# Performance work log

Measured on AMD Instinct MI355X. Metric: run time of the kernel, lower is better.

The kernel has to match this reference:

```python
import jax, jax.numpy as jnp
import numpy as np

D_MODEL = 2048
N_HEADS = 16
D_K = D_MODEL // N_HEADS


def setup_inputs() -> dict:
    key = jax.random.key(0)
    ks = jax.random.split(key, 9)
    s = 1.0 / np.sqrt(D_MODEL)
    def lin(k):
        kw, kb = jax.random.split(k)
        W = jax.random.uniform(kw, (D_MODEL, D_MODEL), jnp.float32, -s, s)
        b = jax.random.uniform(kb, (D_MODEL,), jnp.float32, -s, s)
        return W, b
    Wq, bq = lin(ks[0])
    Wk, bk = lin(ks[1])
    Wv, bv = lin(ks[2])
    Wo, bo = lin(ks[3])
    x = jax.random.normal(ks[4], (2, 2048, D_MODEL), jnp.float32)
    return {"x": x, "Wq": Wq, "bq": bq, "Wk": Wk, "bk": bk,
            "Wv": Wv, "bv": bv, "Wo": Wo, "bo": bo}


def _mha(x, Wq, bq, Wk, bk, Wv, bv, Wo, bo):
    B, S, _ = x.shape
    # Linear projections (torch Linear: x @ W.T + b), split into heads: b s (h d) -> b h s d
    def proj(W, b):
        y = jnp.einsum('bsm,nm->bsn', x, W) + b
        return y.reshape(B, S, N_HEADS, D_K).transpose(0, 2, 1, 3)
    q = proj(Wq, bq)
    k = proj(Wk, bk)
    v = proj(Wv, bv)
    scores = jnp.einsum('bhsd,bhtd->bhst', q, k) / jnp.sqrt(jnp.float32(D_K))
    causal = jnp.triu(jnp.ones((S, S), bool), k=1)  # True above diagonal -> masked
    scores = jnp.where(causal[None, None], -jnp.inf, scores)
    attn = jax.nn.softmax(scores, axis=-1)  # dropout p=0 (eval)
    out = jnp.einsum('bhst,bhtd->bhsd', attn, v)
    out = out.transpose(0, 2, 1, 3).reshape(B, S, D_MODEL)
    return jnp.einsum('bsm,nm->bsn', out, Wo) + bo


def reference(x, Wq, bq, Wk, bk, Wv, bv, Wo, bo):
    return _mha(x, Wq, bq, Wk, bk, Wv, bv, Wo, bo)
```

## Files before the change

### kernel.cpp

```cpp
#include <hip/hip_runtime.h>

typedef unsigned short u16;
typedef __attribute__((ext_vector_type(8))) short bf16x8;
typedef __attribute__((ext_vector_type(4))) float f32x4;
typedef __attribute__((ext_vector_type(4))) unsigned short u16x4;

__device__ __forceinline__ u16 f2bf(float f) {
  union { float f; unsigned u; } v; v.f = f;
  return (u16)((v.u + 0x7FFFu + ((v.u >> 16) & 1u)) >> 16);
}

__device__ __forceinline__ void gload16(const u16* g, u16* l) {
  __builtin_amdgcn_global_load_lds((const __attribute__((address_space(1))) void*)g,
                                   (__attribute__((address_space(3))) void*)l, 16, 0, 0);
}

__global__ __launch_bounds__(256) void k_f2bf5(
    const float* __restrict__ i0, const float* __restrict__ i1, const float* __restrict__ i2,
    const float* __restrict__ i3, const float* __restrict__ i4,
    u16* o0, u16* o1, u16* o2, u16* o3, u16* o4, int n4x, int n4w) {
  const int seg = blockIdx.y;
  const float* in = (seg == 0) ? i0 : (seg == 1) ? i1 : (seg == 2) ? i2 : (seg == 3) ? i3 : i4;
  u16* out = (seg == 0) ? o0 : (seg == 1) ? o1 : (seg == 2) ? o2 : (seg == 3) ? o3 : o4;
  const int n4 = (seg == 0) ? n4x : n4w;
  int i = blockIdx.x * 256 + threadIdx.x;
  const int stride = gridDim.x * 256;
  for (; i < n4; i += stride) {
    const float4 v = ((const float4*)in)[i];
    u16x4 o;
    o.x = f2bf(v.x); o.y = f2bf(v.y); o.z = f2bf(v.z); o.w = f2bf(v.w);
    ((u16x4*)out)[i] = o;
  }
}

template <int OUT_F32>
__global__ __launch_bounds__(256, 4) void k_gemm12(
    const u16* __restrict__ A, const u16* __restrict__ Bt,
    const float* __restrict__ b0, const float* __restrict__ b1, const float* __restrict__ b2,
    u16* __restrict__ C0, u16* __restrict__ C1, u16* __restrict__ C2,
    float* __restrict__ Cf, int NBM)
{
  __shared__ alignas(16) u16 As[8192];
  __shared__ alignas(16) u16 Bs[8192];

  const int tid = threadIdx.x;
  const int lane = tid & 63, wid = tid >> 6;
  const int fr = lane & 15, fg = lane >> 4;
  const int wr = wid >> 1, wc = wid & 1;

  const int nblk = gridDim.x;
  const int q = nblk >> 3, r = nblk & 7;
  const int xcd = blockIdx.x & 7, lid = blockIdx.x >> 3;
  const int wgid = (xcd < r ? xcd * (q + 1) : r * (q + 1) + (xcd - r) * q) + lid;
  const int mb = wgid % NBM, nb = wgid / NBM;
  const long row0 = (long)mb * 128;
  const long col0 = (long)nb * 128;

  int sRow[4], sCol[4];
#pragma unroll
  for (int i = 0; i < 4; ++i) {
    const int g = (wid * 4 + i) * 64 + lane;
    sRow[i] = g >> 3;
    sCol[i] = ((g & 7) ^ (sRow[i] & 7)) << 3;
  }

  const int sw = fr & 7;
  const int aBase = (wr * 64 + fr) * 64;
  const int bBase = (wc * 64 + fr) * 64;
  const int pc0 = (fg ^ sw) << 3;
  const int pc1 = ((4 + fg) ^ sw) << 3;

  f32x4 acc[4][4] = {};

#pragma unroll 1
  for (int t = 0; t < 32; ++t) {
    if (t) __syncthreads();
    const long k0 = (long)t << 6;
#pragma unroll
    for (int i = 0; i < 4; ++i) {
      gload16(A  + (row0 + sRow[i]) * 2048L + k0 + sCol[i], &As[(wid * 4 + i) * 512]);
      gload16(Bt + (col0 + sRow[i]) * 2048L + k0 + sCol[i], &Bs[(wid * 4 + i) * 512]);
    }
    __syncthreads();

#pragma unroll
    for (int kc = 0; kc < 2; ++kc) {
      const int pc = kc ? pc1 : pc0;
      bf16x8 a[4], b[4];
#pragma unroll
      for (int i = 0; i < 4; ++i) {
        a[i] = *(const bf16x8*)&As[aBase + i * 1024 + pc];
        b[i] = *(const bf16x8*)&Bs[bBase + i * 1024 + pc];
      }
#pragma unroll
      for (int i = 0; i < 4; ++i)
#pragma unroll
        for (int j = 0; j < 4; ++j)
          acc[i][j] = __builtin_amdgcn_mfma_f32_16x16x32_bf16(a[i], b[j], acc[i][j], 0, 0, 0);
    }
  }

  const int seg = (int)(col0 >> 11);
  const long colL = col0 & 2047;
  const float* bp = (seg == 0) ? b0 : (seg == 1) ? b1 : b2;
  u16* Cb = (seg == 0) ? C0 : (seg == 1) ? C1 : C2;
#pragma unroll
  for (int j = 0; j < 4; ++j) {
    const long cN = colL + wc * 64 + j * 16 + fr;
    const float bv = bp[cN];
#pragma unroll
    for (int i = 0; i < 4; ++i) {
      const long rM = row0 + wr * 64 + i * 16 + fg * 4;
#pragma unroll
      for (int reg = 0; reg < 4; ++reg) {
        const float v = acc[i][j][reg] + bv;
        if (OUT_F32) Cf[(rM + reg) * 2048 + cN] = v;
        else         Cb[(rM + reg) * 2048 + cN] = f2bf(v);
      }
    }
  }
}

__global__ __launch_bounds__(256) void k_transpose_v(const u16* __restrict__ V,
                                                     u16* __restrict__ Vt) {
  __shared__ u16 t[64][68];
  const int bh = blockIdx.z;
  const long s0 = (long)blockIdx.x * 64;
  const long d0 = (long)blockIdx.y * 64;
  const int tid = threadIdx.x;
  const long rowbase = (long)(bh >> 4) * 2048;
  const int hcol = (bh & 15) * 128;
#pragma unroll
  for (int i = 0; i < 4; ++i) {
    const int v = tid + i * 256;
    const int r = v >> 4, c4 = (v & 15) << 2;
    const u16x4 val = *(const u16x4*)&V[(rowbase + s0 + r) * 2048 + hcol + d0 + c4];
    *(u16x4*)&t[r][c4] = val;
  }
  __syncthreads();
#pragma unroll
  for (int i = 0; i < 4; ++i) {
    const int v = tid + i * 256;
    const int dr = v >> 4, s4 = (v & 15) << 2;
    u16x4 o;
    o.x = t[s4 + 0][dr]; o.y = t[s4 + 1][dr]; o.z = t[s4 + 2][dr]; o.w = t[s4 + 3][dr];
    *(u16x4*)&Vt[((long)bh * 128 + d0 + dr) * 2048 + s0 + s4] = o;
  }
}

__global__ __launch_bounds__(256, 2) void k_flash_attn(
    const u16* __restrict__ Q, const u16* __restrict__ K, const u16* __restrict__ Vt,
    u16* __restrict__ O)
{
  __shared__ alignas(16) u16 Kt[2][8192];
  __shared__ alignas(16) u16 Vtt[2][8192];
  __shared__ alignas(16) u16 Plds[4][16][72];

  const int tid = threadIdx.x;
  const int lane = tid & 63, wid = tid >> 6;
  const int fr = lane & 15, fg = lane >> 4;

  const int L = blockIdx.x;
  const int bh = (L & 7) * 4 + ((L >> 3) & 3);
  const int bx = L >> 5;

  const long rowbase = (long)(bh >> 4) * 2048;
  const int hcol = (bh & 15) * 128;
  const u16* Kg = K + rowbase * 2048 + hcol;
  const u16* Vg = Vt + (long)bh * 128 * 2048;
  const float scale2 = 0.08838834764831845f * 1.44269504089f;

  int kR[4], kC[4], vR[4], vC[4];
#pragma unroll
  for (int i = 0; i < 4; ++i) {
    const int g = (wid * 4 + i) * 64 + lane;
    kR[i] = g >> 4;
    kC[i] = ((g & 15) ^ (kR[i] & 7)) << 3;
    vR[i] = g >> 3;
    vC[i] = ((g & 7) ^ (vR[i] & 7)) << 3;
  }

  const int sw = fr & 7;
  int kbase[4], vbase[2];
#pragma unroll
  for (int c = 0; c < 4; ++c) kbase[c] = fr * 128 + (((c * 4 + fg) ^ sw) << 3);
#pragma unroll
  for (int kc = 0; kc < 2; ++kc) vbase[kc] = fr * 64 + (((kc * 4 + fg) ^ sw) << 3);

  for (int pass = 0; pass < 2; ++pass) {
    const int qblk = pass ? (31 - bx) : bx;
    const int n = qblk + 1;
    const int q_lo = qblk * 64 + wid * 16;
    const int qg = q_lo + fr;

    bf16x8 qf[4];
#pragma unroll
    for (int c = 0; c < 4; ++c)
      qf[c] = *(const bf16x8*)&Q[(rowbase + q_lo + fr) * 2048 + hcol + c * 32 + fg * 8];

    f32x4 oacc[8] = {};
    float m_run = -1e30f, l_run = 0.0f;

#pragma unroll
    for (int i = 0; i < 4; ++i) {
      gload16(Kg + (long)kR[i] * 2048 + kC[i], &Kt[0][(wid * 4 + i) * 512]);
      gload16(Vg + (long)vR[i] * 2048 + vC[i], &Vtt[0][(wid * 4 + i) * 512]);
    }

    int cur = 0;
    for (int j = 0; j < n; ++j) {
      if (j + 1 < n) {
        const long kv = (long)(j + 1) * 64;
#pragma unroll
        for (int i = 0; i < 4; ++i) {
          gload16(Kg + (kv + kR[i]) * 2048 + kC[i], &Kt[cur ^ 1][(wid * 4 + i) * 512]);
          gload16(Vg + (long)vR[i] * 2048 + kv + vC[i], &Vtt[cur ^ 1][(wid * 4 + i) * 512]);
        }
        asm volatile("s_waitcnt vmcnt(8)" ::: "memory");
      } else {
        asm volatile("s_waitcnt vmcnt(0)" ::: "memory");
      }
      __builtin_amdgcn_s_barrier();
      __builtin_amdgcn_sched_barrier(0);

      const int kvlo = j * 64;
      const bool skip = (kvlo >= q_lo + 16);
      if (!skip) {
        const bool needmask = (kvlo + 63 > q_lo);

        f32x4 st[4] = {};
        const u16* kt = Kt[cur];
        __builtin_amdgcn_s_setprio(1);
#pragma unroll
        for (int t = 0; t < 4; ++t)
#pragma unroll
          for (int c = 0; c < 4; ++c) {
            const bf16x8 kf = *(const bf16x8*)&kt[kbase[c] + t * 2048];
            st[t] = __builtin_amdgcn_mfma_f32_16x16x32_bf16(kf, qf[c], st[t], 0, 0, 0);
          }
        __builtin_amdgcn_s_setprio(0);

        float pmax = -1e30f;
        if (needmask) {
#pragma unroll
          for (int t = 0; t < 4; ++t)
#pragma unroll
            for (int r = 0; r < 4; ++r) {
              const int kg = kvlo + t * 16 + fg * 4 + r;
              const float v = (kg <= qg) ? st[t][r] * scale2 : -1e30f;
              st[t][r] = v;
              pmax = fmaxf(pmax, v);
            }
        } else {
#pragma unroll
          for (int t = 0; t < 4; ++t)
#pragma unroll
            for (int r = 0; r < 4; ++r) {
              const float v = st[t][r] * scale2;
              st[t][r] = v;
              pmax = fmaxf(pmax, v);
            }
        }
        pmax = fmaxf(pmax, __shfl_xor(pmax, 16));
        pmax = fmaxf(pmax, __shfl_xor(pmax, 32));

        if (!__all(pmax <= m_run + 8.f)) {
          const float nm = fmaxf(m_run, pmax);
          const float al = exp2f(m_run - nm);
          l_run *= al;
          m_run = nm;
#pragma unroll
          for (int dt = 0; dt < 8; ++dt)
#pragma unroll
            for (int r = 0; r < 4; ++r) oacc[dt][r] *= al;
        }

        float lsum = 0.f;
#pragma unroll
        for (int t = 0; t < 4; ++t)
#pragma unroll
          for (int r = 0; r < 4; ++r) {
            const float p = exp2f(st[t][r] - m_run);
            st[t][r] = p;
            lsum += p;
          }
        lsum += __shfl_xor(lsum, 16);
        lsum += __shfl_xor(lsum, 32);
        l_run += lsum;

#pragma unroll
        for (int t = 0; t < 4; ++t)
#pragma unroll
          for (int r = 0; r < 4; ++r)
            Plds[wid][fr][t * 16 + fg * 4 + r] = f2bf(st[t][r]);
        asm volatile("s_waitcnt lgkmcnt(0)" ::: "memory");
        __builtin_amdgcn_sched_barrier(0);

        const u16* vt = Vtt[cur];
        __builtin_amdgcn_s_setprio(1);
#pragma unroll
        for (int kc = 0; kc < 2; ++kc) {
          const bf16x8 pf = *(const bf16x8*)&Plds[wid][fr][kc * 32 + fg * 8];
#pragma unroll
          for (int dt = 0; dt < 8; ++dt) {
            const bf16x8 vf = *(const bf16x8*)&vt[vbase[kc] + dt * 1024];
            oacc[dt] = __builtin_amdgcn_mfma_f32_16x16x32_bf16(vf, pf, oacc[dt], 0, 0, 0);
          }
        }
        __builtin_amdgcn_s_setprio(0);
      }

      asm volatile("" ::: "memory");
      __builtin_amdgcn_s_barrier();
      cur ^= 1;
    }

    const float linv = 1.0f / l_run;
    const long orow = (rowbase + q_lo + fr) * 2048 + hcol;
#pragma unroll
    for (int dt = 0; dt < 8; ++dt) {
      u16x4 o;
#pragma unroll
      for (int r = 0; r < 4; ++r) o[r] = f2bf(oacc[dt][r] * linv);
      *(u16x4*)&O[orow + dt * 16 + fg * 4] = o;
    }
  }
}

extern "C" void kernel_launch(void* const* d_in, const int* in_sizes, int n_in,
                              void* d_out, int out_size, void* d_ws, size_t ws_size,
                              hipStream_t stream) {
  const float* x  = (const float*)d_in[0];
  const float* Wq = (const float*)d_in[1];
  const float* bq = (const float*)d_in[2];
  const float* Wk = (const float*)d_in[3];
  const float* bk = (const float*)d_in[4];
  const float* Wv = (const float*)d_in[5];
  const float* bv = (const float*)d_in[6];
  const float* Wo = (const float*)d_in[7];
  const float* bo = (const float*)d_in[8];
  float* out = (float*)d_out;

  char* ws = (char*)d_ws;
  const size_t SZ_X = 16777216;
  const size_t SZ_W = 8388608;
  u16* xb  = (u16*)(ws);
  u16* wqb = (u16*)(ws + SZ_X);
  u16* wkb = (u16*)(ws + SZ_X + 1 * SZ_W);
  u16* wvb = (u16*)(ws + SZ_X + 2 * SZ_W);
  u16* wob = (u16*)(ws + SZ_X + 3 * SZ_W);
  u16* Qb  = (u16*)(ws + 1 * SZ_X + 4 * SZ_W);
  u16* Kb  = (u16*)(ws + 2 * SZ_X + 4 * SZ_W);
  u16* Vb  = (u16*)(ws + 3 * SZ_X + 4 * SZ_W);
  u16* Vtb = (u16*)(ws + 4 * SZ_X + 4 * SZ_W);
  u16* Ob  = Vb;

  k_f2bf5<<<dim3(1024, 5), 256, 0, stream>>>(x, Wq, Wk, Wv, Wo,
                                             xb, wqb, wkb, wvb, wob,
                                             8388608 / 4, 4194304 / 4);

  k_gemm12<0><<<1536, 256, 0, stream>>>(xb, wqb, bq, bk, bv, Qb, Kb, Vb, nullptr, 32);

  k_transpose_v<<<dim3(32, 2, 32), 256, 0, stream>>>(Vb, Vtb);

  k_flash_attn<<<512, 256, 0, stream>>>(Qb, Kb, Vtb, Ob);

  k_gemm12<1><<<512, 256, 0, stream>>>(Ob, wob, bo, bo, bo, nullptr, nullptr, nullptr, out, 32);
}
```

Baseline: 261.7 us.

## Use 256x256-tile ping-pong GEMM with 8 waves for fused QKV projection

```diff
diff --git a/kernel.cpp b/kernel.cpp
--- a/kernel.cpp
+++ b/kernel.cpp
@@ -33,6 +33,141 @@
   }
 }
 
+#define RD_A(BUF, mq) do { _Pragma("unroll") \
+  for (int mi = 0; mi < 4; ++mi) { \
+    a[mi][0] = *(const bf16x8*)&(BUF)[aB + ((mq) * 64 + mi * 16) * 64 + pc0]; \
+    a[mi][1] = *(const bf16x8*)&(BUF)[aB + ((mq) * 64 + mi * 16) * 64 + pc1]; } } while (0)
+
+#define RD_B(BUF, BR, nq) do { _Pragma("unroll") \
+  for (int ni = 0; ni < 2; ++ni) { \
+    BR[ni][0] = *(const bf16x8*)&(BUF)[bB + ((nq) * 32 + ni * 16) * 64 + pc0]; \
+    BR[ni][1] = *(const bf16x8*)&(BUF)[bB + ((nq) * 32 + ni * 16) * 64 + pc1]; } } while (0)
+
+#define MM(mq, BR, nq) do { _Pragma("unroll") \
+  for (int kk = 0; kk < 2; ++kk) { _Pragma("unroll") \
+    for (int mi = 0; mi < 4; ++mi) { _Pragma("unroll") \
+      for (int ni = 0; ni < 2; ++ni) \
+        acc[(mq) * 4 + mi][(nq) * 2 + ni] = __builtin_amdgcn_mfma_f32_16x16x32_bf16( \
+            a[mi][kk], BR[ni][kk], acc[(mq) * 4 + mi][(nq) * 2 + ni], 0, 0, 0); } } } while (0)
+
+#define ST_HA0(AN, kofs) do { _Pragma("unroll") \
+  for (int i = 0; i < 2; ++i) \
+    gload16(A + (row0 + rbA1[i] + rl) * 2048L + (kofs) + swc, &(AN)[rbA1[i] * 64]); } while (0)
+#define ST_HA1(AN, kofs) do { _Pragma("unroll") \
+  for (int i = 0; i < 2; ++i) \
+    gload16(A + (row0 + rbA1[i] + 64 + rl) * 2048L + (kofs) + swc, &(AN)[(rbA1[i] + 64) * 64]); } while (0)
+#define ST_HB0(BN_, kofs) do { _Pragma("unroll") \
+  for (int i = 0; i < 2; ++i) \
+    gload16(Bt + (col0 + rbB1[i] + rl) * 2048L + (kofs) + swc, &(BN_)[rbB1[i] * 64]); } while (0)
+#define ST_HB1(BN_, kofs) do { _Pragma("unroll") \
+  for (int i = 0; i < 2; ++i) \
+    gload16(Bt + (col0 + rbB1[i] + 32 + rl) * 2048L + (kofs) + swc, &(BN_)[(rbB1[i] + 32) * 64]); } while (0)
+
+#define WAITV(N) asm volatile("s_waitcnt vmcnt(" #N ")" ::: "memory")
+#define BAR __builtin_amdgcn_s_barrier()
+#define FENCE asm volatile("" ::: "memory")
+#define LGKM0 do { asm volatile("s_waitcnt lgkmcnt(0)" ::: "memory"); \
+  __builtin_amdgcn_sched_barrier(0); } while (0)
+
+#define TILE8(AS, BS, AN, BN_, tn, W1, W2, W4, DOST) do { \
+  const long kofs_ = (long)(tn) << 6; \
+   \
+  RD_A(AS, 0); RD_B(BS, b0f, 0); \
+  if (DOST) ST_HA0(AN, kofs_); \
+  WAITV(W1); BAR; FENCE; LGKM0; \
+  __builtin_amdgcn_s_setprio(1); MM(0, b0f, 0); __builtin_amdgcn_s_setprio(0); \
+  BAR; FENCE; \
+   \
+  RD_B(BS, b1f, 1); \
+  if (DOST) ST_HB0(BN_, kofs_); \
+  WAITV(W2); BAR; FENCE; LGKM0; \
+  __builtin_amdgcn_s_setprio(1); MM(0, b1f, 1); __builtin_amdgcn_s_setprio(0); \
+  BAR; FENCE; \
+   \
+  RD_A(AS, 1); \
+  if (DOST) ST_HB1(BN_, kofs_); \
+  BAR; FENCE; LGKM0; \
+  __builtin_amdgcn_s_setprio(1); MM(1, b1f, 1); __builtin_amdgcn_s_setprio(0); \
+  BAR; FENCE; \
+   \
+  if (DOST) ST_HA1(AN, kofs_); \
+  WAITV(W4); BAR; FENCE; \
+  __builtin_amdgcn_sched_barrier(0); \
+  __builtin_amdgcn_s_setprio(1); MM(1, b0f, 0); __builtin_amdgcn_s_setprio(0); \
+  BAR; FENCE; \
+} while (0)
+
+__global__ __launch_bounds__(512, 1) void k_gemm256ph(
+    const u16* __restrict__ A, const u16* __restrict__ Bt,
+    const float* __restrict__ bias0, const float* __restrict__ bias1,
+    const float* __restrict__ bias2,
+    u16* __restrict__ C0, u16* __restrict__ C1, u16* __restrict__ C2, int NBM)
+{
+  __shared__ alignas(16) u16 As0[16384], Bs0[16384], As1[16384], Bs1[16384];
+
+  const int tid = threadIdx.x;
+  const int lane = tid & 63, wid = tid >> 6;
+  const int fr = lane & 15, fg = lane >> 4;
+  const int wr = wid >> 2, wc = wid & 3;
+
+  const int nblk = gridDim.x;
+  const int q = nblk >> 3, r = nblk & 7;
+  const int xcd = blockIdx.x & 7, lid = blockIdx.x >> 3;
+  const int wgid = (xcd < r ? xcd * (q + 1) : r * (q + 1) + (xcd - r) * q) + lid;
+  const int mb = wgid % NBM, nb = wgid / NBM;
+  const long row0 = (long)mb * 256;
+  const long col0 = (long)nb * 256;
+
+  const int rl = lane >> 3;
+  const int jc = lane & 7;
+  const int swc = (jc ^ rl) << 3;
+  int rbA1[2], rbB1[2];
+#pragma unroll
+  for (int i = 0; i < 2; ++i) {
+    const int S = wid * 2 + i;
+    rbA1[i] = ((S & 7) << 3) | ((S >> 3) << 7);
+    rbB1[i] = ((S >> 2) << 6) | ((S & 3) << 3);
+  }
+
+  const int sw = fr & 7;
+  const int aB = (wr * 128 + fr) * 64;
+  const int bB = (wc * 64 + fr) * 64;
+  const int pc0 = (fg ^ sw) << 3;
+  const int pc1 = ((4 + fg) ^ sw) << 3;
+
+  f32x4 acc[8][4] = {};
+  bf16x8 a[4][2], b0f[2][2], b1f[2][2];
+
+  ST_HA0(As0, 0); ST_HB0(Bs0, 0); ST_HB1(Bs0, 0); ST_HA1(As0, 0);
+  WAITV(0);
+  BAR; FENCE;
+
+#pragma unroll 1
+  for (int t = 0; t < 30; t += 2) {
+    TILE8(As0, Bs0, As1, Bs1, t + 1, 4, 4, 4, true);
+    TILE8(As1, Bs1, As0, Bs0, t + 2, 4, 4, 4, true);
+  }
+  TILE8(As0, Bs0, As1, Bs1, 31, 4, 4, 4, true);
+  TILE8(As1, Bs1, As0, Bs0, 0, 2, 0, 0, false);
+
+  const int seg = (int)(col0 >> 11);
+  const long colL = col0 & 2047;
+  const float* bp = (seg == 0) ? bias0 : (seg == 1) ? bias1 : bias2;
+  u16* Cb = (seg == 0) ? C0 : (seg == 1) ? C1 : C2;
+#pragma unroll
+  for (int n = 0; n < 4; ++n) {
+    const long cN = colL + wc * 64 + (n >> 1) * 32 + (n & 1) * 16 + fr;
+    const float bv = bp[cN];
+#pragma unroll
+    for (int m = 0; m < 8; ++m) {
+      const long rM = row0 + wr * 128 + (m >> 2) * 64 + (m & 3) * 16 + fg * 4;
+#pragma unroll
+      for (int reg = 0; reg < 4; ++reg)
+        Cb[(rM + reg) * 2048 + cN] = f2bf(acc[m][n][reg] + bv);
+    }
+  }
+}
+
 template <int OUT_F32>
 __global__ __launch_bounds__(256, 4) void k_gemm12(
     const u16* __restrict__ A, const u16* __restrict__ Bt,
@@ -359,7 +494,7 @@
                                              xb, wqb, wkb, wvb, wob,
                                              8388608 / 4, 4194304 / 4);
 
-  k_gemm12<0><<<1536, 256, 0, stream>>>(xb, wqb, bq, bk, bv, Qb, Kb, Vb, nullptr, 32);
+  k_gemm256ph<<<384, 512, 0, stream>>>(xb, wqb, bq, bk, bv, Qb, Kb, Vb, 16);
 
   k_transpose_v<<<dim3(32, 2, 32), 256, 0, stream>>>(Vb, Vtb);
 
```

Result: slower. 277.5 us (+6.0%).

## Split flash-attention KV tile across wave pairs with 32-row Q per wave and LDS merge

Applied to the files above, without the earlier changes.

```diff
diff --git a/kernel.cpp b/kernel.cpp
--- a/kernel.cpp
+++ b/kernel.cpp
@@ -152,13 +152,18 @@
     const u16* __restrict__ Q, const u16* __restrict__ K, const u16* __restrict__ Vt,
     u16* __restrict__ O)
 {
-  __shared__ alignas(16) u16 Kt[2][8192];
-  __shared__ alignas(16) u16 Vtt[2][8192];
-  __shared__ alignas(16) u16 Plds[4][16][72];
+  __shared__ alignas(16) u16 SM[38400];
+  u16* Kt  = SM;
+  u16* Vtt = SM + 16384;
+  u16* Pl  = SM + 32768;
+  float* statsM = (float*)(SM + 37888);
+  float* statsL = (float*)(SM + 38144);
+  float* mergeO = (float*)SM;
 
   const int tid = threadIdx.x;
   const int lane = tid & 63, wid = tid >> 6;
   const int fr = lane & 15, fg = lane >> 4;
+  const int kvh = wid >> 1, qh = wid & 1;
 
   const int L = blockIdx.x;
   const int bh = (L & 7) * 4 + ((L >> 3) & 3);
@@ -181,30 +186,34 @@
   }
 
   const int sw = fr & 7;
-  int kbase[4], vbase[2];
-#pragma unroll
-  for (int c = 0; c < 4; ++c) kbase[c] = fr * 128 + (((c * 4 + fg) ^ sw) << 3);
-#pragma unroll
-  for (int kc = 0; kc < 2; ++kc) vbase[kc] = fr * 64 + (((kc * 4 + fg) ^ sw) << 3);
+  int kOff[2][4];
+#pragma unroll
+  for (int kvt = 0; kvt < 2; ++kvt)
+#pragma unroll
+    for (int c = 0; c < 4; ++c)
+      kOff[kvt][c] = kvh * 4096 + kvt * 2048 + fr * 128 + (((c * 4 + fg) ^ sw) << 3);
+  const int vB = fr * 64 + (((kvh * 4 + fg) ^ sw) << 3);
+  const int pBase = wid * 1280;
 
   for (int pass = 0; pass < 2; ++pass) {
     const int qblk = pass ? (31 - bx) : bx;
     const int n = qblk + 1;
-    const int q_lo = qblk * 64 + wid * 16;
-    const int qg = q_lo + fr;
-
-    bf16x8 qf[4];
-#pragma unroll
-    for (int c = 0; c < 4; ++c)
-      qf[c] = *(const bf16x8*)&Q[(rowbase + q_lo + fr) * 2048 + hcol + c * 32 + fg * 8];
-
-    f32x4 oacc[8] = {};
-    float m_run = -1e30f, l_run = 0.0f;
+    const int qw = qblk * 64 + qh * 32;
+
+    bf16x8 qf[2][4];
+#pragma unroll
+    for (int qs = 0; qs < 2; ++qs)
+#pragma unroll
+      for (int c = 0; c < 4; ++c)
+        qf[qs][c] = *(const bf16x8*)&Q[(rowbase + qw + qs * 16 + fr) * 2048 + hcol + c * 32 + fg * 8];
+
+    f32x4 oacc[2][8] = {};
+    float m_run[2] = {-1e30f, -1e30f}, l_run[2] = {0.0f, 0.0f};
 
 #pragma unroll
     for (int i = 0; i < 4; ++i) {
-      gload16(Kg + (long)kR[i] * 2048 + kC[i], &Kt[0][(wid * 4 + i) * 512]);
-      gload16(Vg + (long)vR[i] * 2048 + vC[i], &Vtt[0][(wid * 4 + i) * 512]);
+      gload16(Kg + (long)kR[i] * 2048 + kC[i], &Kt[(wid * 4 + i) * 512]);
+      gload16(Vg + (long)vR[i] * 2048 + vC[i], &Vtt[(wid * 4 + i) * 512]);
     }
 
     int cur = 0;
@@ -213,8 +222,8 @@
         const long kv = (long)(j + 1) * 64;
 #pragma unroll
         for (int i = 0; i < 4; ++i) {
-          gload16(Kg + (kv + kR[i]) * 2048 + kC[i], &Kt[cur ^ 1][(wid * 4 + i) * 512]);
-          gload16(Vg + (long)vR[i] * 2048 + kv + vC[i], &Vtt[cur ^ 1][(wid * 4 + i) * 512]);
+          gload16(Kg + (kv + kR[i]) * 2048 + kC[i], &Kt[(cur ^ 1) * 8192 + (wid * 4 + i) * 512]);
+          gload16(Vg + (long)vR[i] * 2048 + kv + vC[i], &Vtt[(cur ^ 1) * 8192 + (wid * 4 + i) * 512]);
         }
         asm volatile("s_waitcnt vmcnt(8)" ::: "memory");
       } else {
@@ -223,89 +232,109 @@
       __builtin_amdgcn_s_barrier();
       __builtin_amdgcn_sched_barrier(0);
 
-      const int kvlo = j * 64;
-      const bool skip = (kvlo >= q_lo + 16);
+      const int kvbase = j * 64 + kvh * 32;
+      const bool skip = (kvbase >= qw + 32);
       if (!skip) {
-        const bool needmask = (kvlo + 63 > q_lo);
-
-        f32x4 st[4] = {};
-        const u16* kt = Kt[cur];
+        const bool needmask = (kvbase + 31 > qw);
+
+        f32x4 st[2][2] = {};
+        const u16* kt = &Kt[cur * 8192];
         __builtin_amdgcn_s_setprio(1);
 #pragma unroll
-        for (int t = 0; t < 4; ++t)
+        for (int kvt = 0; kvt < 2; ++kvt)
 #pragma unroll
           for (int c = 0; c < 4; ++c) {
-            const bf16x8 kf = *(const bf16x8*)&kt[kbase[c] + t * 2048];
-            st[t] = __builtin_amdgcn_mfma_f32_16x16x32_bf16(kf, qf[c], st[t], 0, 0, 0);
+            const bf16x8 kf = *(const bf16x8*)&kt[kOff[kvt][c]];
+            st[0][kvt] = __builtin_amdgcn_mfma_f32_16x16x32_bf16(kf, qf[0][c], st[0][kvt], 0, 0, 0);
+            st[1][kvt] = __builtin_amdgcn_mfma_f32_16x16x32_bf16(kf, qf[1][c], st[1][kvt], 0, 0, 0);
           }
         __builtin_amdgcn_s_setprio(0);
 
-        float pmax = -1e30f;
+        float pmax[2] = {-1e30f, -1e30f};
         if (needmask) {
 #pragma unroll
-          for (int t = 0; t < 4; ++t)
+          for (int qs = 0; qs < 2; ++qs) {
+            const int qg = qw + qs * 16 + fr;
+#pragma unroll
+            for (int kvt = 0; kvt < 2; ++kvt)
+#pragma unroll
+              for (int r = 0; r < 4; ++r) {
+                const int kg = kvbase + kvt * 16 + fg * 4 + r;
+                const float v = (kg <= qg) ? st[qs][kvt][r] * scale2 : -1e30f;
+                st[qs][kvt][r] = v;
+                pmax[qs] = fmaxf(pmax[qs], v);
+              }
+          }
+        } else {
+#pragma unroll
+          for (int qs = 0; qs < 2; ++qs)
+#pragma unroll
+            for (int kvt = 0; kvt < 2; ++kvt)
+#pragma unroll
+              for (int r = 0; r < 4; ++r) {
+                const float v = st[qs][kvt][r] * scale2;
+                st[qs][kvt][r] = v;
+                pmax[qs] = fmaxf(pmax[qs], v);
+              }
+        }
+#pragma unroll
+        for (int qs = 0; qs < 2; ++qs) {
+          pmax[qs] = fmaxf(pmax[qs], __shfl_xor(pmax[qs], 16));
+          pmax[qs] = fmaxf(pmax[qs], __shfl_xor(pmax[qs], 32));
+        }
+
+        const int ok = (pmax[0] <= m_run[0] + 8.f) & (pmax[1] <= m_run[1] + 8.f);
+        if (!__all(ok)) {
+#pragma unroll
+          for (int qs = 0; qs < 2; ++qs) {
+            const float nm = fmaxf(m_run[qs], pmax[qs]);
+            const float al = exp2f(m_run[qs] - nm);
+            l_run[qs] *= al;
+            m_run[qs] = nm;
+#pragma unroll
+            for (int dt = 0; dt < 8; ++dt)
+#pragma unroll
+              for (int r = 0; r < 4; ++r) oacc[qs][dt][r] *= al;
+          }
+        }
+
+        float lsum[2] = {0.f, 0.f};
+#pragma unroll
+        for (int qs = 0; qs < 2; ++qs)
+#pragma unroll
+          for (int kvt = 0; kvt < 2; ++kvt)
 #pragma unroll
             for (int r = 0; r < 4; ++r) {
-              const int kg = kvlo + t * 16 + fg * 4 + r;
-              const float v = (kg <= qg) ? st[t][r] * scale2 : -1e30f;
-              st[t][r] = v;
-              pmax = fmaxf(pmax, v);
+              const float p = exp2f(st[qs][kvt][r] - m_run[qs]);
+              st[qs][kvt][r] = p;
+              lsum[qs] += p;
             }
-        } else {
-#pragma unroll
-          for (int t = 0; t < 4; ++t)
-#pragma unroll
-            for (int r = 0; r < 4; ++r) {
-              const float v = st[t][r] * scale2;
-              st[t][r] = v;
-              pmax = fmaxf(pmax, v);
-            }
-        }
-        pmax = fmaxf(pmax, __shfl_xor(pmax, 16));
-        pmax = fmaxf(pmax, __shfl_xor(pmax, 32));
-
-        if (!__all(pmax <= m_run + 8.f)) {
-          const float nm = fmaxf(m_run, pmax);
-          const float al = exp2f(m_run - nm);
-          l_run *= al;
-          m_run = nm;
-#pragma unroll
-          for (int dt = 0; dt < 8; ++dt)
-#pragma unroll
-            for (int r = 0; r < 4; ++r) oacc[dt][r] *= al;
-        }
-
-        float lsum = 0.f;
-#pragma unroll
-        for (int t = 0; t < 4; ++t)
-#pragma unroll
-          for (int r = 0; r < 4; ++r) {
-            const float p = exp2f(st[t][r] - m_run);
-            st[t][r] = p;
-            lsum += p;
-          }
-        lsum += __shfl_xor(lsum, 16);
-        lsum += __shfl_xor(lsum, 32);
-        l_run += lsum;
-
-#pragma unroll
-        for (int t = 0; t < 4; ++t)
-#pragma unroll
-          for (int r = 0; r < 4; ++r)
-            Plds[wid][fr][t * 16 + fg * 4 + r] = f2bf(st[t][r]);
+#pragma unroll
+        for (int qs = 0; qs < 2; ++qs) {
+          lsum[qs] += __shfl_xor(lsum[qs], 16);
+          lsum[qs] += __shfl_xor(lsum[qs], 32);
+          l_run[qs] += lsum[qs];
+        }
+
+#pragma unroll
+        for (int qs = 0; qs < 2; ++qs)
+#pragma unroll
+          for (int kvt = 0; kvt < 2; ++kvt)
+#pragma unroll
+            for (int r = 0; r < 4; ++r)
+              Pl[pBase + (qs * 16 + fr) * 40 + kvt * 16 + fg * 4 + r] = f2bf(st[qs][kvt][r]);
         asm volatile("s_waitcnt lgkmcnt(0)" ::: "memory");
         __builtin_amdgcn_sched_barrier(0);
 
-        const u16* vt = Vtt[cur];
+        const u16* vt = &Vtt[cur * 8192];
+        const bf16x8 pf0 = *(const bf16x8*)&Pl[pBase + fr * 40 + fg * 8];
+        const bf16x8 pf1 = *(const bf16x8*)&Pl[pBase + (16 + fr) * 40 + fg * 8];
         __builtin_amdgcn_s_setprio(1);
 #pragma unroll
-        for (int kc = 0; kc < 2; ++kc) {
-          const bf16x8 pf = *(const bf16x8*)&Plds[wid][fr][kc * 32 + fg * 8];
-#pragma unroll
-          for (int dt = 0; dt < 8; ++dt) {
-            const bf16x8 vf = *(const bf16x8*)&vt[vbase[kc] + dt * 1024];
-            oacc[dt] = __builtin_amdgcn_mfma_f32_16x16x32_bf16(vf, pf, oacc[dt], 0, 0, 0);
-          }
+        for (int dt = 0; dt < 8; ++dt) {
+          const bf16x8 vf = *(const bf16x8*)&vt[vB + dt * 1024];
+          oacc[0][dt] = __builtin_amdgcn_mfma_f32_16x16x32_bf16(vf, pf0, oacc[0][dt], 0, 0, 0);
+          oacc[1][dt] = __builtin_amdgcn_mfma_f32_16x16x32_bf16(vf, pf1, oacc[1][dt], 0, 0, 0);
         }
         __builtin_amdgcn_s_setprio(0);
       }
@@ -315,15 +344,53 @@
       cur ^= 1;
     }
 
-    const float linv = 1.0f / l_run;
-    const long orow = (rowbase + q_lo + fr) * 2048 + hcol;
-#pragma unroll
-    for (int dt = 0; dt < 8; ++dt) {
-      u16x4 o;
-#pragma unroll
-      for (int r = 0; r < 4; ++r) o[r] = f2bf(oacc[dt][r] * linv);
-      *(u16x4*)&O[orow + dt * 16 + fg * 4] = o;
-    }
+    if (fg == 0) {
+#pragma unroll
+      for (int qs = 0; qs < 2; ++qs) {
+        statsM[wid * 32 + qs * 16 + fr] = m_run[qs];
+        statsL[wid * 32 + qs * 16 + fr] = l_run[qs];
+      }
+    }
+    __syncthreads();
+    const int pw = wid ^ 2;
+    float aself[2], ltot[2];
+#pragma unroll
+    for (int qs = 0; qs < 2; ++qs) {
+      const float mp = statsM[pw * 32 + qs * 16 + fr];
+      const float lp = statsL[pw * 32 + qs * 16 + fr];
+      const float m = fmaxf(m_run[qs], mp);
+      aself[qs] = exp2f(m_run[qs] - m);
+      const float ap = exp2f(mp - m);
+      ltot[qs] = aself[qs] * l_run[qs] + ap * lp;
+    }
+    if (kvh == 1) {
+#pragma unroll
+      for (int qs = 0; qs < 2; ++qs)
+#pragma unroll
+        for (int dt = 0; dt < 8; ++dt)
+#pragma unroll
+          for (int r = 0; r < 4; ++r)
+            mergeO[qh * 4224 + (qs * 16 + fr) * 132 + dt * 16 + fg * 4 + r] =
+                aself[qs] * oacc[qs][dt][r];
+    }
+    __syncthreads();
+    if (kvh == 0) {
+#pragma unroll
+      for (int qs = 0; qs < 2; ++qs) {
+        const float inv = 1.0f / ltot[qs];
+        const long orow = (rowbase + qw + qs * 16 + fr) * 2048 + hcol;
+#pragma unroll
+        for (int dt = 0; dt < 8; ++dt) {
+          u16x4 o;
+#pragma unroll
+          for (int r = 0; r < 4; ++r)
+            o[r] = f2bf((aself[qs] * oacc[qs][dt][r] +
+                         mergeO[qh * 4224 + (qs * 16 + fr) * 132 + dt * 16 + fg * 4 + r]) * inv);
+          *(u16x4*)&O[orow + dt * 16 + fg * 4] = o;
+        }
+      }
+    }
+    __syncthreads();
   }
 }
 
```

Measured after the change: 260.1 us (median of 2 runs). Within noise of the previous version (-0.6%).
